# Kernel tuning notes

Measured on AMD Instinct MI355X. Metric: run time of the kernel, lower is better.

The kernel has to match this reference:

```python
import jax, jax.numpy as jnp
import numpy as np

EPS = 1e-8  # torch cosine similarity eps


def setup_inputs() -> dict:
    key = jax.random.key(0)
    k1, k2 = jax.random.split(key)
    B, D, H, W = 8, 32, 512, 512
    C = 19
    inputs = jax.random.normal(k1, (B, D, H, W), dtype=jnp.float32)
    targets = jax.random.randint(k2, (B, H, W), 0, C, dtype=jnp.int64)
    return {"inputs": inputs, "targets": targets, "num_classes": C}


def reference(inputs, targets, num_classes):
    C = int(num_classes)
    B, D, H, W = inputs.shape
    # [N, D] pixel embeddings and [N] class labels (N = B*H*W)
    feats = inputs.transpose(0, 2, 3, 1).reshape(-1, D)
    labels = targets.reshape(-1)

    ones = jnp.ones(feats.shape[0], dtype=feats.dtype)
    counts = jax.ops.segment_sum(ones, labels, num_segments=C)          # [C]
    sums = jax.ops.segment_sum(feats, labels, num_segments=C)           # [C, D]
    denom = jnp.maximum(counts, 1.0)                                    # max(mask.sum(), 1)
    centers = sums / denom[:, None]                                     # [C, D] (zeros for absent classes)
    present = counts > 0

    # ---- sim_loss: sum_i mean_{p in class i} (1 - cos(center_i, x_p)) ----
    cnorm = jnp.linalg.norm(centers, axis=1)                            # [C]
    fnorm = jnp.linalg.norm(feats, axis=1)                              # [N]
    dots = jnp.sum(feats * centers[labels], axis=1)                     # [N]
    cos_p = dots / jnp.maximum(fnorm * cnorm[labels], EPS)              # [N]
    seg_cos = jax.ops.segment_sum(cos_p, labels, num_segments=C)        # [C]
    sim_loss = jnp.sum(jnp.where(present, 1.0 - seg_cos / denom, 0.0))

    # ---- diff_loss: sum over present i of mean_j [ (1-cos) if j==i else relu(cos) ] ----
    cosM = (centers @ centers.T) / jnp.maximum(cnorm[:, None] * cnorm[None, :], EPS)  # [C, C]
    eye = jnp.eye(C, dtype=bool)
    terms = jnp.where(eye, 1.0 - cosM, jnp.maximum(cosM, 0.0))
    diff_per_i = jnp.mean(terms, axis=1)                                # CosineEmbeddingLoss mean over C rows
    diff_loss = jnp.sum(jnp.where(present, diff_per_i, 0.0))

    return (sim_loss + diff_loss).reshape(1)  # original returns a shape-[1] tensor
```

## Files before the change

kernel.cpp:

```cpp
#include <hip/hip_runtime.h>

#define BB 8
#define DD 32
#define HH 512
#define WW 512
#define HWSZ (HH*WW)
#define NPIX (BB*HWSZ)
#define CC 19
#define EPSF 1e-8f

#define CSTRIDE 65
#define ACCSZ (CC*CSTRIDE)

#define P 256
#define XSTR 264
#define NT1 256
#define NB1 1024
#define NTILES (NPIX/P)
#define TPB (HWSZ/P)

#define LX_INVN (32*XSTR)
#define LX_LABS (LX_INVN + P)
#define LX_SS   (LX_LABS + P)
#define LTOT    (LX_SS + 1024)

__global__ void k0_zero(float* __restrict__ acc)
{
    int i = blockIdx.x * 256 + threadIdx.x;
    if (i < ACCSZ) acc[i] = 0.f;
}

#define NCB 256
__global__ __launch_bounds__(256) void k_count(const int* __restrict__ tgt,
                                               float* __restrict__ acc)
{
    __shared__ float h[32*20];
    const int t = threadIdx.x;
    for (int i = t; i < 32*20; i += 256) h[i] = 0.f;
    __syncthreads();
    float* my = h + (t & 31) * 20;
    const int T = NCB * 256;
    int tid = blockIdx.x * 256 + t;
    for (int i = tid; i < NPIX/4; i += T) {
        int4 lv = ((const int4*)tgt)[i];
        unsafeAtomicAdd(my + lv.x, 1.f);
        unsafeAtomicAdd(my + lv.y, 1.f);
        unsafeAtomicAdd(my + lv.z, 1.f);
        unsafeAtomicAdd(my + lv.w, 1.f);
    }
    __syncthreads();
    if (t < CC) {
        float s = 0.f;
        #pragma unroll
        for (int k = 0; k < 32; k++) s += h[k*20 + t];
        unsafeAtomicAdd(acc + t*CSTRIDE + 64, s);
    }
}

#define PROC(XX, NN, LL)                                  \
    {                                                     \
        const float x_  = (XX);                           \
        const float xn_ = x_ * (NN);                      \
        const int   l_  = (LL);                           \
        _Pragma("unroll")                                 \
        for (int c = 0; c < CC; c++) {                    \
            const float m_ = (l_ == c) ? 1.0f : 0.0f;     \
            aS[c] = fmaf(m_, x_,  aS[c]);                 \
            aN[c] = fmaf(m_, xn_, aN[c]);                 \
        }                                                 \
    }

__global__ __launch_bounds__(NT1, 4) void k1_accum(
    const float* __restrict__ in, const int* __restrict__ tgt,
    float* __restrict__ acc)
{
    __shared__ __align__(16) float sm[LTOT];
    const int t = threadIdx.x;

    float aS[CC], aN[CC];
    #pragma unroll
    for (int c = 0; c < CC; c++) { aS[c] = 0.f; aN[c] = 0.f; }

    const int dq  = t >> 6;
    const int q   = t & 63;
    const int d   = t >> 3;
    const int sub = t & 7;
    const float* xrow = sm + d * XSTR;

    for (int tl = blockIdx.x; tl < NTILES; tl += gridDim.x) {
        const int b  = tl / TPB;
        const int hw = (tl & (TPB - 1)) * P;
        const float* gb = in + ((size_t)(b*DD + dq*8) * HWSZ) + hw + 4*q;

        if (t < 64) {
            int4 lv = *(const int4*)(tgt + (size_t)tl * P + 4*t);
            *(int4*)((int*)sm + LX_LABS + 4*t) = lv;
        }

        float4 ss = make_float4(0.f, 0.f, 0.f, 0.f);
        #pragma unroll
        for (int dd = 0; dd < 8; dd++) {
            float4 x = *(const float4*)(gb + (size_t)dd * HWSZ);
            ss.x = fmaf(x.x, x.x, ss.x);
            ss.y = fmaf(x.y, x.y, ss.y);
            ss.z = fmaf(x.z, x.z, ss.z);
            ss.w = fmaf(x.w, x.w, ss.w);
            *(float4*)(sm + (dq*8 + dd)*XSTR + 4*q) = x;
        }
        *(float4*)(sm + LX_SS + (dq*64 + q)*4) = ss;
        __syncthreads();

        if (t < 64) {
            float4 s0 = *(const float4*)(sm + LX_SS +        4*t);
            float4 s1 = *(const float4*)(sm + LX_SS + 256  + 4*t);
            float4 s2 = *(const float4*)(sm + LX_SS + 512  + 4*t);
            float4 s3 = *(const float4*)(sm + LX_SS + 768  + 4*t);
            float4 iv;
            iv.x = rsqrtf(fmaxf(s0.x + s1.x + s2.x + s3.x, 1e-30f));
            iv.y = rsqrtf(fmaxf(s0.y + s1.y + s2.y + s3.y, 1e-30f));
            iv.z = rsqrtf(fmaxf(s0.z + s1.z + s2.z + s3.z, 1e-30f));
            iv.w = rsqrtf(fmaxf(s0.w + s1.w + s2.w + s3.w, 1e-30f));
            *(float4*)(sm + LX_INVN + 4*t) = iv;
        }
        __syncthreads();

        #pragma unroll 1
        for (int k = 0; k < P/32; k++) {
            const int p0 = 4*sub + 32*k;
            float4 xv = *(const float4*)(xrow + p0);
            float4 nv = *(const float4*)(sm + LX_INVN + p0);
            int4   lv = *(const int4*)((int*)sm + LX_LABS + p0);
            PROC(xv.x, nv.x, lv.x);
            PROC(xv.y, nv.y, lv.y);
            PROC(xv.z, nv.z, lv.z);
            PROC(xv.w, nv.w, lv.w);
        }
        __syncthreads();
    }

    #pragma unroll
    for (int c = 0; c < CC; c++) {
        sm[t*39 + c]      = aS[c];
        sm[t*39 + 19 + c] = aN[c];
    }
    __syncthreads();
    for (int i = t; i < 32*38; i += NT1) {
        const int dI = i / 38, j = i % 38;
        float s = 0.f;
        #pragma unroll
        for (int su = 0; su < 8; su++) s += sm[(dI*8 + su)*39 + j];
        const int gi = (j < 19) ? (j*CSTRIDE + dI) : ((j - 19)*CSTRIDE + 32 + dI);
        unsafeAtomicAdd(acc + gi, s);
    }
}

__global__ void k3_final(const float* __restrict__ gacc, float* __restrict__ out)
{
    __shared__ float acc[ACCSZ];
    __shared__ float cn[CC];
    __shared__ float pres[CC];
    __shared__ float red[256];
    const int t = threadIdx.x;

    for (int i = t; i < ACCSZ; i += 256) acc[i] = gacc[i];
    __syncthreads();

    float part = 0.f;

    if (t < CC) {
        const float* a = acc + t * CSTRIDE;
        float n2 = 0.f, dotS = 0.f;
        #pragma unroll
        for (int dd = 0; dd < DD; dd++) {
            n2   = fmaf(a[dd], a[dd], n2);
            dotS = fmaf(a[dd], a[32 + dd], dotS);
        }
        float count = a[64];
        float den   = fmaxf(count, 1.f);
        float norm  = sqrtf(n2);
        cn[t]   = norm;
        pres[t] = (count > 0.f) ? 1.f : 0.f;
        float segcos = (norm > 0.f) ? (dotS / norm) : 0.f;
        part += (count > 0.f) ? (1.f - segcos / den) : 0.f;
    }
    __syncthreads();

    for (int p = t; p < CC * CC; p += 256) {
        int i = p / CC, j = p % CC;
        const float* ai = acc + i * CSTRIDE;
        const float* aj = acc + j * CSTRIDE;
        float dot = 0.f;
        #pragma unroll
        for (int dd = 0; dd < DD; dd++) dot = fmaf(ai[dd], aj[dd], dot);
        float ddn  = fmaxf(cn[i] * cn[j], EPSF);
        float cs   = dot / ddn;
        float term = (i == j) ? (1.f - cs) : fmaxf(cs, 0.f);
        part += pres[i] * term * (1.f / (float)CC);
    }

    red[t] = part;
    __syncthreads();
    #pragma unroll
    for (int s = 128; s > 0; s >>= 1) {
        if (t < s) red[t] += red[t + s];
        __syncthreads();
    }
    if (t == 0) out[0] = red[0];
}

extern "C" void kernel_launch(void* const* d_in, const int* in_sizes, int n_in,
                              void* d_out, int out_size, void* d_ws, size_t ws_size,
                              hipStream_t stream)
{
    const float* in  = (const float*)d_in[0];
    const int*   tgt = (const int*)d_in[1];
    float* out = (float*)d_out;
    float* acc = (float*)d_ws;

    hipLaunchKernelGGL(k0_zero,  dim3((ACCSZ + 255) / 256), dim3(256), 0, stream, acc);
    hipLaunchKernelGGL(k_count,  dim3(NCB),  dim3(256), 0, stream, tgt, acc);
    hipLaunchKernelGGL(k1_accum, dim3(NB1),  dim3(256), 0, stream, in, tgt, acc);
    hipLaunchKernelGGL(k3_final, dim3(1),    dim3(256), 0, stream, acc, out);
}
```

Before: 589.4 us.

## Prefetch next tile into registers and compute norms via wave shuffles

```diff
diff --git a/kernel.cpp b/kernel.cpp
--- a/kernel.cpp
+++ b/kernel.cpp
@@ -18,11 +18,11 @@
 #define NB1 1024
 #define NTILES (NPIX/P)
 #define TPB (HWSZ/P)
+#define TILES_PER_BLK (NTILES/NB1)
 
 #define LX_INVN (32*XSTR)
 #define LX_LABS (LX_INVN + P)
-#define LX_SS   (LX_LABS + P)
-#define LTOT    (LX_SS + 1024)
+#define LTOT 9984
 
 __global__ void k0_zero(float* __restrict__ acc)
 {
@@ -30,7 +30,7 @@
     if (i < ACCSZ) acc[i] = 0.f;
 }
 
-#define NCB 256
+#define NCB 1024
 __global__ __launch_bounds__(256) void k_count(const int* __restrict__ tgt,
                                                float* __restrict__ acc)
 {
@@ -75,68 +75,84 @@
     float* __restrict__ acc)
 {
     __shared__ __align__(16) float sm[LTOT];
+    int* const smi = (int*)sm;
     const int t = threadIdx.x;
 
-    float aS[CC], aN[CC];
-    #pragma unroll
-    for (int c = 0; c < CC; c++) { aS[c] = 0.f; aN[c] = 0.f; }
-
-    const int dq  = t >> 6;
-    const int q   = t & 63;
+    const int w  = t >> 6;
+    const int l  = t & 63;
+    const int dq = l & 3;
+    const int q  = l >> 2;
     const int d   = t >> 3;
     const int sub = t & 7;
     const float* xrow = sm + d * XSTR;
 
-    for (int tl = blockIdx.x; tl < NTILES; tl += gridDim.x) {
-        const int b  = tl / TPB;
-        const int hw = (tl & (TPB - 1)) * P;
-        const float* gb = in + ((size_t)(b*DD + dq*8) * HWSZ) + hw + 4*q;
-
-        if (t < 64) {
-            int4 lv = *(const int4*)(tgt + (size_t)tl * P + 4*t);
-            *(int4*)((int*)sm + LX_LABS + 4*t) = lv;
-        }
-
+    float aS[CC], aN[CC];
+    #pragma unroll
+    for (int c = 0; c < CC; c++) { aS[c] = 0.f; aN[c] = 0.f; }
+
+    const int tl0 = blockIdx.x * TILES_PER_BLK;
+    const int b   = tl0 / TPB;
+    const int hw0 = (tl0 % TPB) * P;
+
+    const float* gx = in + ((size_t)(b*DD + dq*8))*HWSZ + hw0 + w*64 + 4*q;
+    const int*   gl = tgt + (size_t)tl0*P + w*64 + 4*q;
+
+    float4 X[8];
+    int4 LB;
+    #pragma unroll
+    for (int dd = 0; dd < 8; dd++) X[dd] = *(const float4*)(gx + (size_t)dd*HWSZ);
+    if (dq == 1) LB = *(const int4*)gl;
+
+    for (int i = 0; i < TILES_PER_BLK; i++) {
         float4 ss = make_float4(0.f, 0.f, 0.f, 0.f);
         #pragma unroll
         for (int dd = 0; dd < 8; dd++) {
-            float4 x = *(const float4*)(gb + (size_t)dd * HWSZ);
-            ss.x = fmaf(x.x, x.x, ss.x);
-            ss.y = fmaf(x.y, x.y, ss.y);
-            ss.z = fmaf(x.z, x.z, ss.z);
-            ss.w = fmaf(x.w, x.w, ss.w);
-            *(float4*)(sm + (dq*8 + dd)*XSTR + 4*q) = x;
-        }
-        *(float4*)(sm + LX_SS + (dq*64 + q)*4) = ss;
+            ss.x = fmaf(X[dd].x, X[dd].x, ss.x);
+            ss.y = fmaf(X[dd].y, X[dd].y, ss.y);
+            ss.z = fmaf(X[dd].z, X[dd].z, ss.z);
+            ss.w = fmaf(X[dd].w, X[dd].w, ss.w);
+        }
+        ss.x += __shfl_xor(ss.x, 1); ss.y += __shfl_xor(ss.y, 1);
+        ss.z += __shfl_xor(ss.z, 1); ss.w += __shfl_xor(ss.w, 1);
+        ss.x += __shfl_xor(ss.x, 2); ss.y += __shfl_xor(ss.y, 2);
+        ss.z += __shfl_xor(ss.z, 2); ss.w += __shfl_xor(ss.w, 2);
+        float4 iv;
+        iv.x = rsqrtf(fmaxf(ss.x, 1e-30f));
+        iv.y = rsqrtf(fmaxf(ss.y, 1e-30f));
+        iv.z = rsqrtf(fmaxf(ss.z, 1e-30f));
+        iv.w = rsqrtf(fmaxf(ss.w, 1e-30f));
+
         __syncthreads();
 
-        if (t < 64) {
-            float4 s0 = *(const float4*)(sm + LX_SS +        4*t);
-            float4 s1 = *(const float4*)(sm + LX_SS + 256  + 4*t);
-            float4 s2 = *(const float4*)(sm + LX_SS + 512  + 4*t);
-            float4 s3 = *(const float4*)(sm + LX_SS + 768  + 4*t);
-            float4 iv;
-            iv.x = rsqrtf(fmaxf(s0.x + s1.x + s2.x + s3.x, 1e-30f));
-            iv.y = rsqrtf(fmaxf(s0.y + s1.y + s2.y + s3.y, 1e-30f));
-            iv.z = rsqrtf(fmaxf(s0.z + s1.z + s2.z + s3.z, 1e-30f));
-            iv.w = rsqrtf(fmaxf(s0.w + s1.w + s2.w + s3.w, 1e-30f));
-            *(float4*)(sm + LX_INVN + 4*t) = iv;
-        }
+        #pragma unroll
+        for (int dd = 0; dd < 8; dd++)
+            *(float4*)(sm + (dq*8 + dd)*XSTR + w*64 + 4*q) = X[dd];
+        if (dq == 0) *(float4*)(sm + LX_INVN + w*64 + 4*q) = iv;
+        if (dq == 1) *(int4*)(smi + LX_LABS + w*64 + 4*q) = LB;
+
         __syncthreads();
 
-        #pragma unroll 1
+        if (i + 1 < TILES_PER_BLK) {
+            gx += P; gl += P;
+            #pragma unroll
+            for (int dd = 0; dd < 8; dd++) X[dd] = *(const float4*)(gx + (size_t)dd*HWSZ);
+            if (dq == 1) LB = *(const int4*)gl;
+        }
+
+        #pragma unroll 2
         for (int k = 0; k < P/32; k++) {
             const int p0 = 4*sub + 32*k;
             float4 xv = *(const float4*)(xrow + p0);
             float4 nv = *(const float4*)(sm + LX_INVN + p0);
-            int4   lv = *(const int4*)((int*)sm + LX_LABS + p0);
+            int4   lv = *(const int4*)(smi + LX_LABS + p0);
             PROC(xv.x, nv.x, lv.x);
             PROC(xv.y, nv.y, lv.y);
             PROC(xv.z, nv.z, lv.z);
             PROC(xv.w, nv.w, lv.w);
         }
-        __syncthreads();
-    }
+    }
+
+    __syncthreads();
 
     #pragma unroll
     for (int c = 0; c < CC; c++) {
```

After: 795.6 us. +35.0%, slower.

## Replace LDS-staged tiles with register-resident per-wave clusters and shuffle norm reduction

Applied to the files above, without the earlier changes.

```diff
diff --git a/kernel.cpp b/kernel.cpp
--- a/kernel.cpp
+++ b/kernel.cpp
@@ -12,17 +12,11 @@
 #define CSTRIDE 65
 #define ACCSZ (CC*CSTRIDE)
 
-#define P 256
-#define XSTR 264
 #define NT1 256
 #define NB1 1024
-#define NTILES (NPIX/P)
-#define TPB (HWSZ/P)
-
-#define LX_INVN (32*XSTR)
-#define LX_LABS (LX_INVN + P)
-#define LX_SS   (LX_LABS + P)
-#define LTOT    (LX_SS + 1024)
+#define CPB 4
+#define CLPX 512
+#define KIT (CLPX/16)
 
 __global__ void k0_zero(float* __restrict__ acc)
 {
@@ -30,7 +24,7 @@
     if (i < ACCSZ) acc[i] = 0.f;
 }
 
-#define NCB 256
+#define NCB 1024
 __global__ __launch_bounds__(256) void k_count(const int* __restrict__ tgt,
                                                float* __restrict__ acc)
 {
@@ -57,99 +51,103 @@
     }
 }
 
-#define PROC(XX, NN, LL)                                  \
-    {                                                     \
-        const float x_  = (XX);                           \
-        const float xn_ = x_ * (NN);                      \
-        const int   l_  = (LL);                           \
-        _Pragma("unroll")                                 \
-        for (int c = 0; c < CC; c++) {                    \
-            const float m_ = (l_ == c) ? 1.0f : 0.0f;     \
-            aS[c] = fmaf(m_, x_,  aS[c]);                 \
-            aN[c] = fmaf(m_, xn_, aN[c]);                 \
-        }                                                 \
-    }
-
-__global__ __launch_bounds__(NT1, 4) void k1_accum(
+#define PROC2(XL, XH, IV, LL)                              \
+    {                                                      \
+        const float xl_ = (XL), xh_ = (XH);                \
+        const float nl_ = xl_ * (IV), nh_ = xh_ * (IV);    \
+        const int   l_  = (LL);                            \
+        _Pragma("unroll")                                  \
+        for (int c = 0; c < CC; c++) {                     \
+            const float m_ = (l_ == c) ? 1.0f : 0.0f;      \
+            aS[c].x = fmaf(m_, xl_, aS[c].x);              \
+            aS[c].y = fmaf(m_, xh_, aS[c].y);              \
+            aN[c].x = fmaf(m_, nl_, aN[c].x);              \
+            aN[c].y = fmaf(m_, nh_, aN[c].y);              \
+        }                                                  \
+    }
+
+__global__ __launch_bounds__(NT1, 2) void k1_accum(
     const float* __restrict__ in, const int* __restrict__ tgt,
     float* __restrict__ acc)
 {
-    __shared__ __align__(16) float sm[LTOT];
-    const int t = threadIdx.x;
-
-    float aS[CC], aN[CC];
-    #pragma unroll
-    for (int c = 0; c < CC; c++) { aS[c] = 0.f; aN[c] = 0.f; }
-
-    const int dq  = t >> 6;
-    const int q   = t & 63;
-    const int d   = t >> 3;
-    const int sub = t & 7;
-    const float* xrow = sm + d * XSTR;
-
-    for (int tl = blockIdx.x; tl < NTILES; tl += gridDim.x) {
-        const int b  = tl / TPB;
-        const int hw = (tl & (TPB - 1)) * P;
-        const float* gb = in + ((size_t)(b*DD + dq*8) * HWSZ) + hw + 4*q;
-
-        if (t < 64) {
-            int4 lv = *(const int4*)(tgt + (size_t)tl * P + 4*t);
-            *(int4*)((int*)sm + LX_LABS + 4*t) = lv;
-        }
-
-        float4 ss = make_float4(0.f, 0.f, 0.f, 0.f);
-        #pragma unroll
-        for (int dd = 0; dd < 8; dd++) {
-            float4 x = *(const float4*)(gb + (size_t)dd * HWSZ);
-            ss.x = fmaf(x.x, x.x, ss.x);
-            ss.y = fmaf(x.y, x.y, ss.y);
-            ss.z = fmaf(x.z, x.z, ss.z);
-            ss.w = fmaf(x.w, x.w, ss.w);
-            *(float4*)(sm + (dq*8 + dd)*XSTR + 4*q) = x;
-        }
-        *(float4*)(sm + LX_SS + (dq*64 + q)*4) = ss;
-        __syncthreads();
-
-        if (t < 64) {
-            float4 s0 = *(const float4*)(sm + LX_SS +        4*t);
-            float4 s1 = *(const float4*)(sm + LX_SS + 256  + 4*t);
-            float4 s2 = *(const float4*)(sm + LX_SS + 512  + 4*t);
-            float4 s3 = *(const float4*)(sm + LX_SS + 768  + 4*t);
-            float4 iv;
-            iv.x = rsqrtf(fmaxf(s0.x + s1.x + s2.x + s3.x, 1e-30f));
-            iv.y = rsqrtf(fmaxf(s0.y + s1.y + s2.y + s3.y, 1e-30f));
-            iv.z = rsqrtf(fmaxf(s0.z + s1.z + s2.z + s3.z, 1e-30f));
-            iv.w = rsqrtf(fmaxf(s0.w + s1.w + s2.w + s3.w, 1e-30f));
-            *(float4*)(sm + LX_INVN + 4*t) = iv;
-        }
-        __syncthreads();
-
-        #pragma unroll 1
-        for (int k = 0; k < P/32; k++) {
-            const int p0 = 4*sub + 32*k;
-            float4 xv = *(const float4*)(xrow + p0);
-            float4 nv = *(const float4*)(sm + LX_INVN + p0);
-            int4   lv = *(const int4*)((int*)sm + LX_LABS + p0);
-            PROC(xv.x, nv.x, lv.x);
-            PROC(xv.y, nv.y, lv.y);
-            PROC(xv.z, nv.z, lv.z);
-            PROC(xv.w, nv.w, lv.w);
-        }
-        __syncthreads();
-    }
-
+    __shared__ float red[CPB*16*76];
+    const int t  = threadIdx.x;
+    const int w  = t >> 6;
+    const int l  = t & 63;
+    const int dp = l >> 2;
+    const int sl = l & 3;
+
+    float2 aS[CC], aN[CC];
     #pragma unroll
     for (int c = 0; c < CC; c++) {
-        sm[t*39 + c]      = aS[c];
-        sm[t*39 + 19 + c] = aN[c];
-    }
-    __syncthreads();
-    for (int i = t; i < 32*38; i += NT1) {
-        const int dI = i / 38, j = i % 38;
-        float s = 0.f;
-        #pragma unroll
-        for (int su = 0; su < 8; su++) s += sm[(dI*8 + su)*39 + j];
-        const int gi = (j < 19) ? (j*CSTRIDE + dI) : ((j - 19)*CSTRIDE + 32 + dI);
+        aS[c] = make_float2(0.f, 0.f);
+        aN[c] = make_float2(0.f, 0.f);
+    }
+
+    const int cluster = (blockIdx.x << 2) | w;
+    const int p0 = cluster << 9;
+    const int b  = p0 >> 18;
+    const int hw = p0 & (HWSZ - 1);
+
+    const float* pl = in + ((size_t)(b*DD + 2*dp))*HWSZ + hw + 4*sl;
+    const float* ph = pl + HWSZ;
+    const int*   pt = tgt + p0 + 4*sl;
+
+    #pragma unroll 1
+    for (int k = 0; k < KIT; k++) {
+        const int o = 16*k;
+        float4 xl = *(const float4*)(pl + o);
+        float4 xh = *(const float4*)(ph + o);
+        int4   lv = *(const int4*)(pt + o);
+
+        float4 ss;
+        ss.x = fmaf(xl.x, xl.x, xh.x*xh.x);
+        ss.y = fmaf(xl.y, xl.y, xh.y*xh.y);
+        ss.z = fmaf(xl.z, xl.z, xh.z*xh.z);
+        ss.w = fmaf(xl.w, xl.w, xh.w*xh.w);
+        #pragma unroll
+        for (int m = 4; m <= 32; m <<= 1) {
+            ss.x += __shfl_xor(ss.x, m);
+            ss.y += __shfl_xor(ss.y, m);
+            ss.z += __shfl_xor(ss.z, m);
+            ss.w += __shfl_xor(ss.w, m);
+        }
+        float4 iv;
+        iv.x = rsqrtf(fmaxf(ss.x, 1e-30f));
+        iv.y = rsqrtf(fmaxf(ss.y, 1e-30f));
+        iv.z = rsqrtf(fmaxf(ss.z, 1e-30f));
+        iv.w = rsqrtf(fmaxf(ss.w, 1e-30f));
+
+        PROC2(xl.x, xh.x, iv.x, lv.x);
+        PROC2(xl.y, xh.y, iv.y, lv.y);
+        PROC2(xl.z, xh.z, iv.z, lv.z);
+        PROC2(xl.w, xh.w, iv.w, lv.w);
+    }
+
+    #pragma unroll
+    for (int c = 0; c < CC; c++) {
+        aS[c].x += __shfl_xor(aS[c].x, 1); aS[c].x += __shfl_xor(aS[c].x, 2);
+        aS[c].y += __shfl_xor(aS[c].y, 1); aS[c].y += __shfl_xor(aS[c].y, 2);
+        aN[c].x += __shfl_xor(aN[c].x, 1); aN[c].x += __shfl_xor(aN[c].x, 2);
+        aN[c].y += __shfl_xor(aN[c].y, 1); aN[c].y += __shfl_xor(aN[c].y, 2);
+    }
+    if (sl == 0) {
+        float* dst = red + (w*16 + dp)*76;
+        #pragma unroll
+        for (int c = 0; c < CC; c++) {
+            dst[c]      = aS[c].x;
+            dst[19 + c] = aS[c].y;
+            dst[38 + c] = aN[c].x;
+            dst[57 + c] = aN[c].y;
+        }
+    }
+    __syncthreads();
+
+    for (int i = t; i < 16*76; i += NT1) {
+        float s = red[i] + red[1216 + i] + red[2432 + i] + red[3648 + i];
+        const int dpi = i / 76, j = i % 76;
+        const int c = j % 19, part = j / 19;
+        const int gi = c*CSTRIDE + 2*dpi + (part & 1) + ((part >= 2) ? 32 : 0);
         unsafeAtomicAdd(acc + gi, s);
     }
 }
```

Result: slower. 642.3 us (+9.0%).
